# Optimization experiments

Measured on AMD Instinct MI355X. Metric: run time of the kernel, lower is better.

## Reference

```python
import jax, jax.numpy as jnp
import numpy as np

N, H, L, OUT = 1048576, 128, 16, 2


def setup_inputs() -> dict:
    key = jax.random.key(0)
    k0, k1, k2, k3, k4 = jax.random.split(key, 5)
    s = 1.0 / np.sqrt(H)  # torch nn.Linear default init bound
    x = jax.random.normal(k0, (N, H), dtype=jnp.float32)
    W = jax.random.uniform(k1, (L, H, H), dtype=jnp.float32, minval=-s, maxval=s)
    b = jax.random.uniform(k2, (L, H), dtype=jnp.float32, minval=-s, maxval=s)
    Wout = jax.random.uniform(k3, (OUT, H), dtype=jnp.float32, minval=-s, maxval=s)
    bout = jax.random.uniform(k4, (OUT,), dtype=jnp.float32, minval=-s, maxval=s)
    return {"x": x, "W": W, "b": b, "Wout": Wout, "bout": bout}


def reference(x, W, b, Wout, bout):
    # layer weights; torch Linear convention: y = x @ W.T + b (W is [out,in]).
    def step(h, wb):
        w, bias = wb
        return jax.nn.relu(h @ w.T + bias), None

    h, _ = jax.lax.scan(step, x, (W, b))
    return h @ Wout.T + bout  # final Linear(128, 2)
```

## Files before the change

### kernel.cpp

```cpp
#include <hip/hip_runtime.h>


#define LAYERS 16
#define SLD    132

typedef __bf16 bf16x8 __attribute__((ext_vector_type(8)));
typedef float  f32x4  __attribute__((ext_vector_type(4)));

__device__ __forceinline__ unsigned short f2bf(float f) {
  unsigned u = __float_as_uint(f);
  u += 0x7fffu + ((u >> 16) & 1u);
  return (unsigned short)(u >> 16);
}

#if __has_builtin(__builtin_amdgcn_cvt_pk_bf16_f32)
typedef __bf16 bf16x2 __attribute__((ext_vector_type(2)));
__device__ __forceinline__ unsigned pkbf(float a, float b) {
  return __builtin_bit_cast(unsigned, __builtin_amdgcn_cvt_pk_bf16_f32(a, b));
}
#else
__device__ __forceinline__ unsigned pkbf(float a, float b) {
  return (((unsigned)f2bf(b)) << 16) | (unsigned)f2bf(a);
}
#endif

__device__ __forceinline__ void split2(float a, float b, unsigned &hw, unsigned &lw) {
  unsigned hp = pkbf(a, b);
  float la = a - __uint_as_float(hp << 16);
  float lb = b - __uint_as_float(hp & 0xffff0000u);
  hw = hp;
  lw = pkbf(la, lb);
}

__device__ __forceinline__ float upk(unsigned w) {
  return __uint_as_float(w & 0xffff0000u) + __uint_as_float(w << 16);
}

__global__ void prep_w(const float* __restrict__ W, unsigned* __restrict__ wf) {
  int t = blockIdx.x * 256 + threadIdx.x;
  int l     = t >> 14;
  int r     = t & 16383;
  int fi    = r >> 8;
  int inner = r & 255;
  int lanei = inner >> 2;
  int d     = inner & 3;
  int term  = fi & 1;
  int ntks  = fi >> 1;
  int nt = ntks >> 2, ks = ntks & 3;
  int n = nt * 16 + (lanei & 15);
  int k = ks * 32 + (lanei >> 4) * 8 + d * 2;
  const float* wp = W + ((l * 128 + n) * 128 + k);
  float w0 = wp[0], w1 = wp[1];
  unsigned hp = pkbf(w0, w1);
  unsigned res;
  if (term == 0) {
    res = hp;
  } else {
    float h0 = __uint_as_float(hp << 16);
    float h1 = __uint_as_float(hp & 0xffff0000u);
    res = pkbf(w0 - h0, w1 - h1);
  }
  wf[t] = res;
}

__launch_bounds__(256, 1)
__global__ void mlp_kernel(const unsigned* __restrict__ wf,
                           const float* __restrict__ bias,
                           const float* __restrict__ x,
                           const float* __restrict__ wout,
                           const float* __restrict__ bout,
                           float* __restrict__ out) {
  __shared__ unsigned sS[4 * 64 * SLD];
  const int tid  = threadIdx.x;
  const int wave = tid >> 6;
  const int lane = tid & 63;
  const int c    = lane & 15;
  const int q    = lane >> 4;
  const int s    = (c >> 2) & 3;
  const long rowbase = (long)blockIdx.x * 256 + wave * 64;

  unsigned* sw = sS + wave * (64 * SLD);

  uint4 a_hi[4][4];
  uint4 a_lo[4][4];

  uint4 bhb[2][4], blb[2][4];
  {
    const uint4* wl0 = (const uint4*)wf;
#pragma unroll
    for (int ks = 0; ks < 4; ++ks) {
      bhb[0][ks] = wl0[((0 * 4 + ks) * 2 + 0) * 64 + lane];
      blb[0][ks] = wl0[((0 * 4 + ks) * 2 + 1) * 64 + lane];
    }
  }
  float bv[8], bv_n[8];
#pragma unroll
  for (int nt = 0; nt < 8; ++nt) bv[nt] = bias[nt * 16 + c];

  {
    const float* xb = x + rowbase * 128;
#pragma unroll
    for (int mt = 0; mt < 4; ++mt) {
      const float* xr = xb + (mt * 16 + c) * 128 + q * 8;
#pragma unroll
      for (int ks = 0; ks < 4; ++ks) {
        float4 v0 = *(const float4*)(xr + ks * 32);
        float4 v1 = *(const float4*)(xr + ks * 32 + 4);
        uint4 hh, ll;
        split2(v0.x, v0.y, hh.x, ll.x);
        split2(v0.z, v0.w, hh.y, ll.y);
        split2(v1.x, v1.y, hh.z, ll.z);
        split2(v1.z, v1.w, hh.w, ll.w);
        a_hi[mt][ks] = hh;
        a_lo[mt][ks] = ll;
      }
    }
  }

#pragma unroll 1
  for (int l = 0; l < LAYERS; ++l) {
    if (l > 0) {
#pragma unroll
      for (int mt = 0; mt < 4; ++mt) {
        const unsigned* rowp = sw + (mt * 16 + c) * SLD;
#pragma unroll
        for (int ks = 0; ks < 4; ++ks) {
          int fb = ks * 32 + 8 * (q ^ s);
          uint4 p0 = *(const uint4*)(rowp + fb);
          uint4 p1 = *(const uint4*)(rowp + fb + 4);
          uint4 hh, ll;
          hh.x = __builtin_amdgcn_perm(p0.y, p0.x, 0x07060302u);
          ll.x = __builtin_amdgcn_perm(p0.y, p0.x, 0x05040100u);
          hh.y = __builtin_amdgcn_perm(p0.w, p0.z, 0x07060302u);
          ll.y = __builtin_amdgcn_perm(p0.w, p0.z, 0x05040100u);
          hh.z = __builtin_amdgcn_perm(p1.y, p1.x, 0x07060302u);
          ll.z = __builtin_amdgcn_perm(p1.y, p1.x, 0x05040100u);
          hh.w = __builtin_amdgcn_perm(p1.w, p1.z, 0x07060302u);
          ll.w = __builtin_amdgcn_perm(p1.w, p1.z, 0x05040100u);
          a_hi[mt][ks] = hh;
          a_lo[mt][ks] = ll;
        }
      }
    }

    const uint4* wl      = (const uint4*)(wf + l * 16384);
    const uint4* wl_next = (const uint4*)(wf + (l + 1) * 16384);

#pragma unroll
    for (int nt = 0; nt < 8; ++nt) {
      const uint4* bh = bhb[nt & 1];
      const uint4* bl = blb[nt & 1];
      uint4* bh_n = bhb[(nt + 1) & 1];
      uint4* bl_n = blb[(nt + 1) & 1];
      if (nt < 7) {
#pragma unroll
        for (int ks = 0; ks < 4; ++ks) {
          bh_n[ks] = wl[(((nt + 1) * 4 + ks) * 2 + 0) * 64 + lane];
          bl_n[ks] = wl[(((nt + 1) * 4 + ks) * 2 + 1) * 64 + lane];
        }
      } else if (l < LAYERS - 1) {
#pragma unroll
        for (int ks = 0; ks < 4; ++ks) {
          bh_n[ks] = wl_next[((0 * 4 + ks) * 2 + 0) * 64 + lane];
          bl_n[ks] = wl_next[((0 * 4 + ks) * 2 + 1) * 64 + lane];
        }
      }
      if (nt == 0 && l < LAYERS - 1) {
#pragma unroll
        for (int j = 0; j < 8; ++j) bv_n[j] = bias[(l + 1) * 128 + j * 16 + c];
      }

      f32x4 acc[4];
#pragma unroll
      for (int mt = 0; mt < 4; ++mt) {
        f32x4 a0 = {bv[nt], bv[nt], bv[nt], bv[nt]};
        acc[mt] = a0;
      }
#pragma unroll
      for (int ks = 0; ks < 4; ++ks) {
        bf16x8 Bh = __builtin_bit_cast(bf16x8, bh[ks]);
        bf16x8 Bl = __builtin_bit_cast(bf16x8, bl[ks]);
#pragma unroll
        for (int mt = 0; mt < 4; ++mt) {
          bf16x8 Ah = __builtin_bit_cast(bf16x8, a_hi[mt][ks]);
          bf16x8 Al = __builtin_bit_cast(bf16x8, a_lo[mt][ks]);
          acc[mt] = __builtin_amdgcn_mfma_f32_16x16x32_bf16(Ah, Bh, acc[mt], 0, 0, 0);
          acc[mt] = __builtin_amdgcn_mfma_f32_16x16x32_bf16(Ah, Bl, acc[mt], 0, 0, 0);
          acc[mt] = __builtin_amdgcn_mfma_f32_16x16x32_bf16(Al, Bh, acc[mt], 0, 0, 0);
        }
      }
#pragma unroll
      for (int mt = 0; mt < 4; ++mt) {
        int fsw = (nt * 16 + c) ^ (8 * q);
        unsigned* wp = sw + (mt * 16 + q * 4) * SLD + fsw;
        float e0 = fmaxf(acc[mt][0], 0.0f);
        float e1 = fmaxf(acc[mt][1], 0.0f);
        float e2 = fmaxf(acc[mt][2], 0.0f);
        float e3 = fmaxf(acc[mt][3], 0.0f);
        unsigned hp, lp, hp2, lp2;
        split2(e0, e1, hp, lp);
        split2(e2, e3, hp2, lp2);
        wp[0 * SLD] = (hp << 16) | (lp & 0xffffu);
        wp[1 * SLD] = (hp & 0xffff0000u) | (lp >> 16);
        wp[2 * SLD] = (hp2 << 16) | (lp2 & 0xffffu);
        wp[3 * SLD] = (hp2 & 0xffff0000u) | (lp2 >> 16);
      }
    }
#pragma unroll
    for (int j = 0; j < 8; ++j) bv[j] = bv_n[j];
  }

  float bo0 = bout[0], bo1 = bout[1];
#pragma unroll
  for (int mt = 0; mt < 4; ++mt) {
    const unsigned* rowp = sw + (mt * 16 + c) * SLD;
    float s0 = 0.0f, s1 = 0.0f;
#pragma unroll
    for (int bb = 0; bb < 4; ++bb) {
      int fpb = q * 32 + bb * 8;
      int fab = q * 32 + (bb ^ s) * 8;
      uint4 h0 = *(const uint4*)(rowp + fpb);
      uint4 h1 = *(const uint4*)(rowp + fpb + 4);
      float4 w00 = *(const float4*)(wout + fab);
      float4 w01 = *(const float4*)(wout + fab + 4);
      float4 w10 = *(const float4*)(wout + 128 + fab);
      float4 w11 = *(const float4*)(wout + 128 + fab + 4);
      float xv;
      xv = upk(h0.x); s0 = fmaf(xv, w00.x, s0); s1 = fmaf(xv, w10.x, s1);
      xv = upk(h0.y); s0 = fmaf(xv, w00.y, s0); s1 = fmaf(xv, w10.y, s1);
      xv = upk(h0.z); s0 = fmaf(xv, w00.z, s0); s1 = fmaf(xv, w10.z, s1);
      xv = upk(h0.w); s0 = fmaf(xv, w00.w, s0); s1 = fmaf(xv, w10.w, s1);
      xv = upk(h1.x); s0 = fmaf(xv, w01.x, s0); s1 = fmaf(xv, w11.x, s1);
      xv = upk(h1.y); s0 = fmaf(xv, w01.y, s0); s1 = fmaf(xv, w11.y, s1);
      xv = upk(h1.z); s0 = fmaf(xv, w01.z, s0); s1 = fmaf(xv, w11.z, s1);
      xv = upk(h1.w); s0 = fmaf(xv, w01.w, s0); s1 = fmaf(xv, w11.w, s1);
    }
    s0 += __shfl_xor(s0, 16); s0 += __shfl_xor(s0, 32);
    s1 += __shfl_xor(s1, 16); s1 += __shfl_xor(s1, 32);
    if (q == 0) {
      long r = rowbase + mt * 16 + c;
      float2 o;
      o.x = s0 + bo0;
      o.y = s1 + bo1;
      *(float2*)(out + r * 2) = o;
    }
  }
}

extern "C" void kernel_launch(void* const* d_in, const int* in_sizes, int n_in,
                              void* d_out, int out_size, void* d_ws, size_t ws_size,
                              hipStream_t stream) {
  (void)in_sizes; (void)n_in; (void)out_size; (void)ws_size;
  const float* x    = (const float*)d_in[0];
  const float* W    = (const float*)d_in[1];
  const float* b    = (const float*)d_in[2];
  const float* wout = (const float*)d_in[3];
  const float* bout = (const float*)d_in[4];
  float* out = (float*)d_out;
  unsigned* wf = (unsigned*)d_ws;

  prep_w<<<dim3(1024), dim3(256), 0, stream>>>(W, wf);
  mlp_kernel<<<dim3(4096), dim3(256), 0, stream>>>(wf, b, x, wout, bout, out);
}
```

Measured before the change: 2.179 ms.

## Keep layer activations in registers by computing transposed MFMA output

Swaps the MFMA operand order so weights are the A operand and activations the B operand. Each lane's accumulator then lines up with the K layout the next layer's input fragment needs, and the weight prep permutes K to match. This removes the per-layer shared-memory round trip of the split bf16 hi/lo activations, along with its permutes, and the final Linear is done straight from the accumulators. The cost is much higher register pressure: 32 accumulator vectors plus two sets of hi/lo activation fragments per wave. That may cause spills or a worse schedule at 256 threads per block.

Measured after the change: 2.776 ms. 1.27x slower.

```diff
diff --git a/kernel.cpp b/kernel.cpp
--- a/kernel.cpp
+++ b/kernel.cpp
@@ -2,7 +2,6 @@
 
 
 #define LAYERS 16
-#define SLD    132
 
 typedef __bf16 bf16x8 __attribute__((ext_vector_type(8)));
 typedef float  f32x4  __attribute__((ext_vector_type(4)));
@@ -30,10 +29,6 @@
   float lb = b - __uint_as_float(hp & 0xffff0000u);
   hw = hp;
   lw = pkbf(la, lb);
-}
-
-__device__ __forceinline__ float upk(unsigned w) {
-  return __uint_as_float(w & 0xffff0000u) + __uint_as_float(w << 16);
 }
 
 __global__ void prep_w(const float* __restrict__ W, unsigned* __restrict__ wf) {
@@ -48,7 +43,8 @@
   int ntks  = fi >> 1;
   int nt = ntks >> 2, ks = ntks & 3;
   int n = nt * 16 + (lanei & 15);
-  int k = ks * 32 + (lanei >> 4) * 8 + d * 2;
+  int q = lanei >> 4;
+  int k = ks * 32 + (d >> 1) * 16 + q * 4 + (d & 1) * 2;
   const float* wp = W + ((l * 128 + n) * 128 + k);
   float w0 = wp[0], w1 = wp[1];
   unsigned hp = pkbf(w0, w1);
@@ -70,170 +66,150 @@
                            const float* __restrict__ wout,
                            const float* __restrict__ bout,
                            float* __restrict__ out) {
-  __shared__ unsigned sS[4 * 64 * SLD];
-  const int tid  = threadIdx.x;
-  const int wave = tid >> 6;
-  const int lane = tid & 63;
+  const int lane = threadIdx.x & 63;
+  const int wave = threadIdx.x >> 6;
   const int c    = lane & 15;
   const int q    = lane >> 4;
-  const int s    = (c >> 2) & 3;
   const long rowbase = (long)blockIdx.x * 256 + wave * 64;
 
-  unsigned* sw = sS + wave * (64 * SLD);
-
-  uint4 a_hi[4][4];
-  uint4 a_lo[4][4];
-
+  uint4 aHi[4][4], aLo[4][4];
+  uint4 nHi[4][4], nLo[4][4];
+  f32x4 acc[8][4];
   uint4 bhb[2][4], blb[2][4];
+  f32x4 bvq[2];
+
   {
     const uint4* wl0 = (const uint4*)wf;
 #pragma unroll
     for (int ks = 0; ks < 4; ++ks) {
-      bhb[0][ks] = wl0[((0 * 4 + ks) * 2 + 0) * 64 + lane];
-      blb[0][ks] = wl0[((0 * 4 + ks) * 2 + 1) * 64 + lane];
-    }
-  }
-  float bv[8], bv_n[8];
-#pragma unroll
-  for (int nt = 0; nt < 8; ++nt) bv[nt] = bias[nt * 16 + c];
+      bhb[0][ks] = wl0[(ks * 2 + 0) * 64 + lane];
+      blb[0][ks] = wl0[(ks * 2 + 1) * 64 + lane];
+    }
+  }
+  bvq[0] = *(const f32x4*)(bias + q * 4);
 
   {
     const float* xb = x + rowbase * 128;
 #pragma unroll
     for (int mt = 0; mt < 4; ++mt) {
-      const float* xr = xb + (mt * 16 + c) * 128 + q * 8;
+      const float* xr = xb + (mt * 16 + c) * 128 + q * 4;
 #pragma unroll
       for (int ks = 0; ks < 4; ++ks) {
-        float4 v0 = *(const float4*)(xr + ks * 32);
-        float4 v1 = *(const float4*)(xr + ks * 32 + 4);
+        f32x4 v0 = *(const f32x4*)(xr + ks * 32);
+        f32x4 v1 = *(const f32x4*)(xr + ks * 32 + 16);
         uint4 hh, ll;
-        split2(v0.x, v0.y, hh.x, ll.x);
-        split2(v0.z, v0.w, hh.y, ll.y);
-        split2(v1.x, v1.y, hh.z, ll.z);
-        split2(v1.z, v1.w, hh.w, ll.w);
-        a_hi[mt][ks] = hh;
-        a_lo[mt][ks] = ll;
+        split2(v0[0], v0[1], hh.x, ll.x);
+        split2(v0[2], v0[3], hh.y, ll.y);
+        split2(v1[0], v1[1], hh.z, ll.z);
+        split2(v1[2], v1[3], hh.w, ll.w);
+        aHi[mt][ks] = hh;
+        aLo[mt][ks] = ll;
       }
     }
   }
 
+#define MLP_LAYER(lv, AIH, AIL, DO_PACK)                                       \
+  {                                                                            \
+    const int _l = (lv);                                                       \
+    const uint4* wl = (const uint4*)(wf) + (size_t)_l * 4096;                  \
+    _Pragma("unroll")                                                          \
+    for (int nt = 0; nt < 8; ++nt) {                                           \
+      {                                                                        \
+        f32x4 ini = bvq[nt & 1];   \
+        _Pragma("unroll")                                                      \
+        for (int mt = 0; mt < 4; ++mt) acc[nt][mt] = ini;                      \
+      }                                                                        \
+               \
+      if (nt < 7) {                                                            \
+        bvq[(nt + 1) & 1] =                                                    \
+            *(const f32x4*)(bias + _l * 128 + (nt + 1) * 16 + q * 4);          \
+        _Pragma("unroll")                                                      \
+        for (int ks = 0; ks < 4; ++ks) {                                       \
+          bhb[(nt + 1) & 1][ks] = wl[(((nt + 1) * 4 + ks) * 2 + 0) * 64 + lane]; \
+          blb[(nt + 1) & 1][ks] = wl[(((nt + 1) * 4 + ks) * 2 + 1) * 64 + lane]; \
+        }                                                                      \
+      } else if (_l < LAYERS - 1) {                                            \
+        bvq[0] = *(const f32x4*)(bias + (_l + 1) * 128 + q * 4);               \
+        _Pragma("unroll")                                                      \
+        for (int ks = 0; ks < 4; ++ks) {                                       \
+          bhb[0][ks] = wl[4096 + (ks * 2 + 0) * 64 + lane];                    \
+          blb[0][ks] = wl[4096 + (ks * 2 + 1) * 64 + lane];                    \
+        }                                                                      \
+      }                                                                        \
+                 \
+      _Pragma("unroll")                                                        \
+      for (int ks = 0; ks < 4; ++ks) {                                         \
+        bf16x8 Wh = __builtin_bit_cast(bf16x8, bhb[nt & 1][ks]);               \
+        bf16x8 Wl = __builtin_bit_cast(bf16x8, blb[nt & 1][ks]);               \
+        _Pragma("unroll")                                                      \
+        for (int mt = 0; mt < 4; ++mt)                                         \
+          acc[nt][mt] = __builtin_amdgcn_mfma_f32_16x16x32_bf16(               \
+              Wh, __builtin_bit_cast(bf16x8, AIH[mt][ks]), acc[nt][mt], 0, 0, 0); \
+        _Pragma("unroll")                                                      \
+        for (int mt = 0; mt < 4; ++mt)                                         \
+          acc[nt][mt] = __builtin_amdgcn_mfma_f32_16x16x32_bf16(               \
+              Wl, __builtin_bit_cast(bf16x8, AIH[mt][ks]), acc[nt][mt], 0, 0, 0); \
+        _Pragma("unroll")                                                      \
+        for (int mt = 0; mt < 4; ++mt)                                         \
+          acc[nt][mt] = __builtin_amdgcn_mfma_f32_16x16x32_bf16(               \
+              Wh, __builtin_bit_cast(bf16x8, AIL[mt][ks]), acc[nt][mt], 0, 0, 0); \
+      }                                                                        \
+           \
+      if ((DO_PACK) && (nt & 1)) {                                             \
+        const int kso = nt >> 1;                                               \
+        _Pragma("unroll")                                                      \
+        for (int mt = 0; mt < 4; ++mt) {                                       \
+          float e0 = fmaxf(acc[nt - 1][mt][0], 0.0f);                          \
+          float e1 = fmaxf(acc[nt - 1][mt][1], 0.0f);                          \
+          float e2 = fmaxf(acc[nt - 1][mt][2], 0.0f);                          \
+          float e3 = fmaxf(acc[nt - 1][mt][3], 0.0f);                          \
+          float f0 = fmaxf(acc[nt][mt][0], 0.0f);                              \
+          float f1 = fmaxf(acc[nt][mt][1], 0.0f);                              \
+          float f2 = fmaxf(acc[nt][mt][2], 0.0f);                              \
+          float f3 = fmaxf(acc[nt][mt][3], 0.0f);                              \
+          uint4 hh, ll;                                                        \
+          split2(e0, e1, hh.x, ll.x);                                          \
+          split2(e2, e3, hh.y, ll.y);                                          \
+          split2(f0, f1, hh.z, ll.z);                                          \
+          split2(f2, f3, hh.w, ll.w);                                          \
+          nHi[mt][kso] = hh;                                                   \
+          nLo[mt][kso] = ll;                                                   \
+        }                                                                      \
+      }                                                                        \
+    }                                                                          \
+  }
+
 #pragma unroll 1
-  for (int l = 0; l < LAYERS; ++l) {
-    if (l > 0) {
-#pragma unroll
-      for (int mt = 0; mt < 4; ++mt) {
-        const unsigned* rowp = sw + (mt * 16 + c) * SLD;
-#pragma unroll
-        for (int ks = 0; ks < 4; ++ks) {
-          int fb = ks * 32 + 8 * (q ^ s);
-          uint4 p0 = *(const uint4*)(rowp + fb);
-          uint4 p1 = *(const uint4*)(rowp + fb + 4);
-          uint4 hh, ll;
-          hh.x = __builtin_amdgcn_perm(p0.y, p0.x, 0x07060302u);
-          ll.x = __builtin_amdgcn_perm(p0.y, p0.x, 0x05040100u);
-          hh.y = __builtin_amdgcn_perm(p0.w, p0.z, 0x07060302u);
-          ll.y = __builtin_amdgcn_perm(p0.w, p0.z, 0x05040100u);
-          hh.z = __builtin_amdgcn_perm(p1.y, p1.x, 0x07060302u);
-          ll.z = __builtin_amdgcn_perm(p1.y, p1.x, 0x05040100u);
-          hh.w = __builtin_amdgcn_perm(p1.w, p1.z, 0x07060302u);
-          ll.w = __builtin_amdgcn_perm(p1.w, p1.z, 0x05040100u);
-          a_hi[mt][ks] = hh;
-          a_lo[mt][ks] = ll;
-        }
+  for (int l = 0; l < LAYERS - 1; ++l) {
+    MLP_LAYER(l, aHi, aLo, 1);
+#pragma unroll
+    for (int mt = 0; mt < 4; ++mt)
+#pragma unroll
+      for (int ks = 0; ks < 4; ++ks) {
+        aHi[mt][ks] = nHi[mt][ks];
+        aLo[mt][ks] = nLo[mt][ks];
       }
-    }
-
-    const uint4* wl      = (const uint4*)(wf + l * 16384);
-    const uint4* wl_next = (const uint4*)(wf + (l + 1) * 16384);
-
+  }
+  MLP_LAYER(LAYERS - 1, aHi, aLo, 0);
+
+  f32x4 wo0[8], wo1[8];
+#pragma unroll
+  for (int nt = 0; nt < 8; ++nt) {
+    wo0[nt] = *(const f32x4*)(wout + nt * 16 + q * 4);
+    wo1[nt] = *(const f32x4*)(wout + 128 + nt * 16 + q * 4);
+  }
+  float bo0 = bout[0], bo1 = bout[1];
+#pragma unroll
+  for (int mt = 0; mt < 4; ++mt) {
+    float s0 = 0.0f, s1 = 0.0f;
 #pragma unroll
     for (int nt = 0; nt < 8; ++nt) {
-      const uint4* bh = bhb[nt & 1];
-      const uint4* bl = blb[nt & 1];
-      uint4* bh_n = bhb[(nt + 1) & 1];
-      uint4* bl_n = blb[(nt + 1) & 1];
-      if (nt < 7) {
-#pragma unroll
-        for (int ks = 0; ks < 4; ++ks) {
-          bh_n[ks] = wl[(((nt + 1) * 4 + ks) * 2 + 0) * 64 + lane];
-          bl_n[ks] = wl[(((nt + 1) * 4 + ks) * 2 + 1) * 64 + lane];
-        }
-      } else if (l < LAYERS - 1) {
-#pragma unroll
-        for (int ks = 0; ks < 4; ++ks) {
-          bh_n[ks] = wl_next[((0 * 4 + ks) * 2 + 0) * 64 + lane];
-          bl_n[ks] = wl_next[((0 * 4 + ks) * 2 + 1) * 64 + lane];
-        }
+#pragma unroll
+      for (int r = 0; r < 4; ++r) {
+        float v = fmaxf(acc[nt][mt][r], 0.0f);
+        s0 = fmaf(v, wo0[nt][r], s0);
+        s1 = fmaf(v, wo1[nt][r], s1);
       }
-      if (nt == 0 && l < LAYERS - 1) {
-#pragma unroll
-        for (int j = 0; j < 8; ++j) bv_n[j] = bias[(l + 1) * 128 + j * 16 + c];
-      }
-
-      f32x4 acc[4];
-#pragma unroll
-      for (int mt = 0; mt < 4; ++mt) {
-        f32x4 a0 = {bv[nt], bv[nt], bv[nt], bv[nt]};
-        acc[mt] = a0;
-      }
-#pragma unroll
-      for (int ks = 0; ks < 4; ++ks) {
-        bf16x8 Bh = __builtin_bit_cast(bf16x8, bh[ks]);
-        bf16x8 Bl = __builtin_bit_cast(bf16x8, bl[ks]);
-#pragma unroll
-        for (int mt = 0; mt < 4; ++mt) {
-          bf16x8 Ah = __builtin_bit_cast(bf16x8, a_hi[mt][ks]);
-          bf16x8 Al = __builtin_bit_cast(bf16x8, a_lo[mt][ks]);
-          acc[mt] = __builtin_amdgcn_mfma_f32_16x16x32_bf16(Ah, Bh, acc[mt], 0, 0, 0);
-          acc[mt] = __builtin_amdgcn_mfma_f32_16x16x32_bf16(Ah, Bl, acc[mt], 0, 0, 0);
-          acc[mt] = __builtin_amdgcn_mfma_f32_16x16x32_bf16(Al, Bh, acc[mt], 0, 0, 0);
-        }
-      }
-#pragma unroll
-      for (int mt = 0; mt < 4; ++mt) {
-        int fsw = (nt * 16 + c) ^ (8 * q);
-        unsigned* wp = sw + (mt * 16 + q * 4) * SLD + fsw;
-        float e0 = fmaxf(acc[mt][0], 0.0f);
-        float e1 = fmaxf(acc[mt][1], 0.0f);
-        float e2 = fmaxf(acc[mt][2], 0.0f);
-        float e3 = fmaxf(acc[mt][3], 0.0f);
-        unsigned hp, lp, hp2, lp2;
-        split2(e0, e1, hp, lp);
-        split2(e2, e3, hp2, lp2);
-        wp[0 * SLD] = (hp << 16) | (lp & 0xffffu);
-        wp[1 * SLD] = (hp & 0xffff0000u) | (lp >> 16);
-        wp[2 * SLD] = (hp2 << 16) | (lp2 & 0xffffu);
-        wp[3 * SLD] = (hp2 & 0xffff0000u) | (lp2 >> 16);
-      }
-    }
-#pragma unroll
-    for (int j = 0; j < 8; ++j) bv[j] = bv_n[j];
-  }
-
-  float bo0 = bout[0], bo1 = bout[1];
-#pragma unroll
-  for (int mt = 0; mt < 4; ++mt) {
-    const unsigned* rowp = sw + (mt * 16 + c) * SLD;
-    float s0 = 0.0f, s1 = 0.0f;
-#pragma unroll
-    for (int bb = 0; bb < 4; ++bb) {
-      int fpb = q * 32 + bb * 8;
-      int fab = q * 32 + (bb ^ s) * 8;
-      uint4 h0 = *(const uint4*)(rowp + fpb);
-      uint4 h1 = *(const uint4*)(rowp + fpb + 4);
-      float4 w00 = *(const float4*)(wout + fab);
-      float4 w01 = *(const float4*)(wout + fab + 4);
-      float4 w10 = *(const float4*)(wout + 128 + fab);
-      float4 w11 = *(const float4*)(wout + 128 + fab + 4);
-      float xv;
-      xv = upk(h0.x); s0 = fmaf(xv, w00.x, s0); s1 = fmaf(xv, w10.x, s1);
-      xv = upk(h0.y); s0 = fmaf(xv, w00.y, s0); s1 = fmaf(xv, w10.y, s1);
-      xv = upk(h0.z); s0 = fmaf(xv, w00.z, s0); s1 = fmaf(xv, w10.z, s1);
-      xv = upk(h0.w); s0 = fmaf(xv, w00.w, s0); s1 = fmaf(xv, w10.w, s1);
-      xv = upk(h1.x); s0 = fmaf(xv, w01.x, s0); s1 = fmaf(xv, w11.x, s1);
-      xv = upk(h1.y); s0 = fmaf(xv, w01.y, s0); s1 = fmaf(xv, w11.y, s1);
-      xv = upk(h1.z); s0 = fmaf(xv, w01.z, s0); s1 = fmaf(xv, w11.z, s1);
-      xv = upk(h1.w); s0 = fmaf(xv, w01.w, s0); s1 = fmaf(xv, w11.w, s1);
     }
     s0 += __shfl_xor(s0, 16); s0 += __shfl_xor(s0, 32);
     s1 += __shfl_xor(s1, 16); s1 += __shfl_xor(s1, 32);
```
